# Optimization experiments

Hardware: AMD Instinct MI355X
Metric: run time of the kernel (lower is better)

Reference implementation:

```python
import math
import jax, jax.numpy as jnp
import numpy as np

B, T, C = 4, 2048, 1024
H = 16
D = C // H  # head dim = 64


def setup_inputs() -> dict:
    key = jax.random.key(0)
    ks = jax.random.split(key, 9)
    s = 0.02
    return {
        "x": jax.random.normal(ks[0], (B, T, C), dtype=jnp.float32),
        "Wq": jax.random.normal(ks[1], (C, C), dtype=jnp.float32) * s,
        "bq": jax.random.normal(ks[2], (C,), dtype=jnp.float32) * s,
        "Wk": jax.random.normal(ks[3], (C, C), dtype=jnp.float32) * s,
        "bk": jax.random.normal(ks[4], (C,), dtype=jnp.float32) * s,
        "Wv": jax.random.normal(ks[5], (C, C), dtype=jnp.float32) * s,
        "bv": jax.random.normal(ks[6], (C,), dtype=jnp.float32) * s,
        "Wo": jax.random.normal(ks[7], (C, C), dtype=jnp.float32) * s,
        "bo": jax.random.normal(ks[8], (C,), dtype=jnp.float32) * s,
    }


def reference(x, Wq, bq, Wk, bk, Wv, bv, Wo, bo):
    # Linear projections (torch Linear: x @ W.T + b), split into heads -> [B,H,T,D]
    def heads(y):
        return y.reshape(B, T, H, D).transpose(0, 2, 1, 3)

    q = heads(x @ Wq.T + bq)
    k = heads(x @ Wk.T + bk)
    v = heads(x @ Wv.T + bv)

    # Full [B,H,T,T] score matrix, scaled by 1/sqrt(D) (no mask, dropout=0 / eval)
    scores = jnp.einsum("bhqd,bhkd->bhqk", q, k) / math.sqrt(D)
    attn = jax.nn.softmax(scores, axis=-1)
    out = jnp.einsum("bhqk,bhkd->bhqd", attn, v)
    out = out.transpose(0, 2, 1, 3).reshape(B, T, C)
    return out @ Wo.T + bo
```

## Files before the change

kernel.cpp:

```cpp
#include <hip/hip_runtime.h>
#include <hip/hip_bf16.h>
#include <stdint.h>

#define Bb 4
#define Tt 2048
#define Cc 1024
#define Hh 16
#define Dd 64

using bf16x8 = __bf16 __attribute__((ext_vector_type(8)));
using f32x4  = float  __attribute__((ext_vector_type(4)));
using f32x2  = float  __attribute__((ext_vector_type(2)));
typedef short s16x4 __attribute__((ext_vector_type(4)));
typedef unsigned short u16;
typedef unsigned int   u32;

#if defined(__has_builtin) && __has_builtin(__builtin_amdgcn_mfma_f32_16x16x16bf16_1k)
#define MFMA_16x16x16_BF16(a, b, c) __builtin_amdgcn_mfma_f32_16x16x16bf16_1k(a, b, c, 0, 0, 0)
#else
static __device__ __forceinline__ f32x4 mfma16x16x16bf16_asm(s16x4 a, s16x4 b, f32x4 c) {
  f32x4 d;
  asm volatile("v_mfma_f32_16x16x16_bf16 %0, %1, %2, %3" : "=v"(d) : "v"(a), "v"(b), "v"(c));
  return d;
}
#define MFMA_16x16x16_BF16(a, b, c) mfma16x16x16bf16_asm(a, b, c)
#endif

#if defined(__has_builtin) && __has_builtin(__builtin_amdgcn_exp2f)
#define EXP2F(x) __builtin_amdgcn_exp2f(x)
#else
#define EXP2F(x) exp2f(x)
#endif

__device__ __forceinline__ u16 f32_to_bf16(float f) {
  union { float f; unsigned u; } v; v.f = f;
  unsigned r = v.u + 0x7fffu + ((v.u >> 16) & 1u);
  return (u16)(r >> 16);
}

__device__ __forceinline__ void gl2lds16(const u16* g, u16* l) {
  __builtin_amdgcn_global_load_lds(
      (const __attribute__((address_space(1))) u32*)g,
      (__attribute__((address_space(3))) u32*)l, 16, 0, 0);
}

__global__ void cast_f32_to_bf16(const float* __restrict__ in, u16* __restrict__ out, int n) {
  int i = (blockIdx.x * blockDim.x + threadIdx.x) * 4;
  if (i >= n) return;
  float4 v = *reinterpret_cast<const float4*>(in + i);
  ushort4 o;
  o.x = f32_to_bf16(v.x); o.y = f32_to_bf16(v.y);
  o.z = f32_to_bf16(v.z); o.w = f32_to_bf16(v.w);
  *reinterpret_cast<ushort4*>(out + i) = o;
}

__global__ void cast4_f32_to_bf16(const float* __restrict__ w0, const float* __restrict__ w1,
                                  const float* __restrict__ w2, const float* __restrict__ w3,
                                  u16* __restrict__ o0, u16* __restrict__ o1,
                                  u16* __restrict__ o2, u16* __restrict__ o3, int n) {
  const float* in; u16* out;
  switch (blockIdx.y) {
    case 0: in = w0; out = o0; break;
    case 1: in = w1; out = o1; break;
    case 2: in = w2; out = o2; break;
    default: in = w3; out = o3; break;
  }
  int i = (blockIdx.x * blockDim.x + threadIdx.x) * 4;
  if (i >= n) return;
  float4 v = *reinterpret_cast<const float4*>(in + i);
  ushort4 o;
  o.x = f32_to_bf16(v.x); o.y = f32_to_bf16(v.y);
  o.z = f32_to_bf16(v.z); o.w = f32_to_bf16(v.w);
  *reinterpret_cast<ushort4*>(out + i) = o;
}

__global__ __launch_bounds__(256, 2)
void gemm_qkv(const u16* __restrict__ A, const u16* __restrict__ Bqkv,
              const float* __restrict__ bq, const float* __restrict__ bk,
              const float* __restrict__ bv,
              u16* __restrict__ qout, u16* __restrict__ kout, u16* __restrict__ vtout,
              float qscl)
{
  constexpr int K = Cc, BK = 32, LDT = 136;
  __shared__ alignas(16) u16 smem[128 * LDT];
  u16* As = smem;
  u16* Bs = smem + 128 * BK;
  const int tid  = threadIdx.x;
  const int wave = tid >> 6, lane = tid & 63;
  const int row0 = blockIdx.x * 128, col0 = blockIdx.y * 128;
  const int seg  = col0 >> 10;
  const int wm = (wave & 1) * 64, wn = (wave >> 1) * 64;
  const int fr = lane & 15, fk = (lane >> 4) * 8;
  const int srow = lane >> 2, scol = (lane & 3) * 8;

  f32x4 acc[4][4] = {};

  for (int k0 = 0; k0 < K; k0 += BK) {
#pragma unroll
    for (int c = 0; c < 2; ++c) {
      int rg = (wave * 2 + c) * 16;
      gl2lds16(A    + (size_t)(row0 + rg + srow) * K + k0 + scol, &As[rg * BK]);
      gl2lds16(Bqkv + (size_t)(col0 + rg + srow) * K + k0 + scol, &Bs[rg * BK]);
    }
    __syncthreads();
    bf16x8 af[4], bf[4];
#pragma unroll
    for (int i = 0; i < 4; ++i) {
      af[i] = *reinterpret_cast<const bf16x8*>(&As[(wm + i * 16 + fr) * BK + fk]);
      bf[i] = *reinterpret_cast<const bf16x8*>(&Bs[(wn + i * 16 + fr) * BK + fk]);
    }
#pragma unroll
    for (int i = 0; i < 4; ++i)
#pragma unroll
      for (int j = 0; j < 4; ++j)
        acc[i][j] = __builtin_amdgcn_mfma_f32_16x16x32_bf16(af[i], bf[j], acc[i][j], 0, 0, 0);
    __syncthreads();
  }

  const float* bias = (seg == 0) ? bq : ((seg == 1) ? bk : bv);
  const float scale = (seg == 0) ? qscl : 1.0f;
  const int colL0 = col0 & 1023;

  if (seg < 2) {
    u16* outp = (seg == 0) ? qout : kout;
#pragma unroll
    for (int j = 0; j < 4; ++j) {
      int col = colL0 + wn + j * 16 + fr;
      float bvv = bias[col];
#pragma unroll
      for (int i = 0; i < 4; ++i) {
        int rowb = row0 + wm + i * 16 + (lane >> 4) * 4;
#pragma unroll
        for (int r = 0; r < 4; ++r)
          outp[(size_t)(rowb + r) * Cc + col] = f32_to_bf16((acc[i][j][r] + bvv) * scale);
      }
    }
  } else {
#pragma unroll
    for (int j = 0; j < 4; ++j) {
      int lc = wn + j * 16 + fr;
      float bvv = bias[colL0 + lc];
#pragma unroll
      for (int i = 0; i < 4; ++i) {
        int lr = wm + i * 16 + (lane >> 4) * 4;
#pragma unroll
        for (int r = 0; r < 4; ++r)
          smem[lc * LDT + lr + r] = f32_to_bf16(acc[i][j][r] + bvv);
      }
    }
    __syncthreads();
    int lc = tid >> 1, seg2 = tid & 1;
    int col = colL0 + lc;
    int h = col >> 6, d = col & 63;
    int bb = row0 >> 11, t0 = (row0 & 2047) + seg2 * 64;
    u16* dst = vtout + ((size_t)(bb * Hh + h) * Dd + d) * Tt + t0;
    const u16* src = &smem[lc * LDT + seg2 * 64];
#pragma unroll
    for (int g = 0; g < 8; ++g)
      *reinterpret_cast<uint4*>(dst + g * 8) = *reinterpret_cast<const uint4*>(src + g * 8);
  }
}

__global__ __launch_bounds__(256, 2)
void gemm_out(const u16* __restrict__ A, const u16* __restrict__ Bw,
              const float* __restrict__ bias, float* __restrict__ Cout,
              int M, int N, int K)
{
  constexpr int BK = 32;
  __shared__ alignas(16) u16 As[128 * BK];
  __shared__ alignas(16) u16 Bs[128 * BK];
  const int tid  = threadIdx.x;
  const int wave = tid >> 6, lane = tid & 63;
  const int row0 = blockIdx.x * 128, col0 = blockIdx.y * 128;
  const int wm = (wave & 1) * 64, wn = (wave >> 1) * 64;
  const int fr = lane & 15, fk = (lane >> 4) * 8;
  const int srow = lane >> 2, scol = (lane & 3) * 8;

  f32x4 acc[4][4] = {};

  for (int k0 = 0; k0 < K; k0 += BK) {
#pragma unroll
    for (int c = 0; c < 2; ++c) {
      int rg = (wave * 2 + c) * 16;
      gl2lds16(A  + (size_t)(row0 + rg + srow) * K + k0 + scol, &As[rg * BK]);
      gl2lds16(Bw + (size_t)(col0 + rg + srow) * K + k0 + scol, &Bs[rg * BK]);
    }
    __syncthreads();
    bf16x8 af[4], bf[4];
#pragma unroll
    for (int i = 0; i < 4; ++i) {
      af[i] = *reinterpret_cast<const bf16x8*>(&As[(wm + i * 16 + fr) * BK + fk]);
      bf[i] = *reinterpret_cast<const bf16x8*>(&Bs[(wn + i * 16 + fr) * BK + fk]);
    }
#pragma unroll
    for (int i = 0; i < 4; ++i)
#pragma unroll
      for (int j = 0; j < 4; ++j)
        acc[i][j] = __builtin_amdgcn_mfma_f32_16x16x32_bf16(af[i], bf[j], acc[i][j], 0, 0, 0);
    __syncthreads();
  }

#pragma unroll
  for (int j = 0; j < 4; ++j) {
    int col = col0 + wn + j * 16 + fr;
    float bv = bias[col];
#pragma unroll
    for (int i = 0; i < 4; ++i) {
      int rowb = row0 + wm + i * 16 + (lane >> 4) * 4;
#pragma unroll
      for (int r = 0; r < 4; ++r)
        Cout[(size_t)(rowb + r) * N + col] = acc[i][j][r] + bv;
    }
  }
}

__global__ __launch_bounds__(256, 2)
void attn_kernel(const u16* __restrict__ Q, const u16* __restrict__ Kmat,
                 const u16* __restrict__ VT, u16* __restrict__ O) {
  constexpr int LDK = 72, LDV = 72;
  __shared__ alignas(16) unsigned char smem[18432];
  u16* Ks = (u16*)smem;
  u16* Vs = (u16*)(smem + 9216);
  float* Of = (float*)smem;
  float* Qs = (float*)(smem + 17408);
  const int tid = threadIdx.x, wave = tid >> 6, lane = tid & 63;
  const int bh = blockIdx.x, qt = blockIdx.y;
  const int b = bh >> 4, h = bh & 15;
  const size_t base = (size_t)b * Tt * Cc + (size_t)h * Dd;
  const int fr = lane & 15, qd = lane >> 4;

  bf16x8 bq0[4], bq1[4];
#pragma unroll
  for (int nb = 0; nb < 4; ++nb) {
    const u16* qp = Q + base + (size_t)(qt * 64 + nb * 16 + fr) * Cc + qd * 8;
    bq0[nb] = *reinterpret_cast<const bf16x8*>(qp);
    bq1[nb] = *reinterpret_cast<const bf16x8*>(qp + 32);
  }

  f32x4 Oacc[4][4] = {};
  f32x2 sacc2[4] = {};
  const size_t vtb = (size_t)bh * Dd * Tt;
  const int sr = tid >> 3, sc = (tid & 7) * 8;

  for (int kt = 0; kt < Tt; kt += 64) {
#pragma unroll
    for (int it = 0; it < 2; ++it) {
      int r = it * 32 + sr;
      *reinterpret_cast<uint4*>(&Ks[r * LDK + sc]) =
          *reinterpret_cast<const uint4*>(Kmat + base + (size_t)(kt + r) * Cc + sc);
      *reinterpret_cast<uint4*>(&Vs[r * LDV + sc]) =
          *reinterpret_cast<const uint4*>(VT + vtb + (size_t)r * Tt + kt + sc);
    }
    __syncthreads();

    bf16x8 ka = *reinterpret_cast<const bf16x8*>(&Ks[(wave * 16 + fr) * LDK + qd * 8]);
    bf16x8 kb = *reinterpret_cast<const bf16x8*>(&Ks[(wave * 16 + fr) * LDK + 32 + qd * 8]);
    s16x4 va[4];
#pragma unroll
    for (int n = 0; n < 4; ++n)
      va[n] = *reinterpret_cast<const s16x4*>(&Vs[(n * 16 + fr) * LDV + wave * 16 + qd * 4]);

    s16x4 pf[4];
#pragma unroll
    for (int nb = 0; nb < 4; ++nb) {
      f32x4 z = {};
      z = __builtin_amdgcn_mfma_f32_16x16x32_bf16(ka, bq0[nb], z, 0, 0, 0);
      f32x4 st = __builtin_amdgcn_mfma_f32_16x16x32_bf16(kb, bq1[nb], z, 0, 0, 0);
      float p0 = EXP2F(st[0]), p1 = EXP2F(st[1]);
      float p2 = EXP2F(st[2]), p3 = EXP2F(st[3]);
      sacc2[nb] += (f32x2){p0, p1} + (f32x2){p2, p3};
      union { __hip_bfloat162 h2; short2 s2; } u01, u23;
      u01.h2 = __float22bfloat162_rn(make_float2(p0, p1));
      u23.h2 = __float22bfloat162_rn(make_float2(p2, p3));
      s16x4 pv; pv[0] = u01.s2.x; pv[1] = u01.s2.y;
      pv[2] = u23.s2.x; pv[3] = u23.s2.y;
      pf[nb] = pv;
    }

#pragma unroll
    for (int n = 0; n < 4; ++n)
#pragma unroll
      for (int nb = 0; nb < 4; ++nb)
        Oacc[n][nb] = MFMA_16x16x16_BF16(va[n], pf[nb], Oacc[n][nb]);

    __syncthreads();
  }

#pragma unroll
  for (int nb = 0; nb < 4; ++nb) {
    float s = sacc2[nb][0] + sacc2[nb][1];
    s += __shfl_xor(s, 16, 64);
    s += __shfl_xor(s, 32, 64);
    if (qd == 0) Qs[wave * 64 + nb * 16 + fr] = s;
  }
  for (int w = 0; w < 4; ++w) {
    if (wave == w) {
#pragma unroll
      for (int n = 0; n < 4; ++n)
#pragma unroll
        for (int nb = 0; nb < 4; ++nb) {
          float* dst = &Of[(nb * 16 + fr) * 68 + n * 16 + qd * 4];
          if (w == 0) *reinterpret_cast<f32x4*>(dst) = Oacc[n][nb];
          else {
            f32x4 old = *reinterpret_cast<const f32x4*>(dst);
            *reinterpret_cast<f32x4*>(dst) = old + Oacc[n][nb];
          }
        }
    }
    __syncthreads();
  }

  {
    int q = tid >> 2, dg = tid & 3;
    float qtot = Qs[q] + Qs[64 + q] + Qs[128 + q] + Qs[192 + q];
    float linv = 1.0f / qtot;
    const float* src = &Of[q * 68 + dg * 16];
    alignas(16) u16 tmp[16];
#pragma unroll
    for (int i = 0; i < 16; ++i) tmp[i] = f32_to_bf16(src[i] * linv);
    u16* op = O + base + (size_t)(qt * 64 + q) * Cc + dg * 16;
    *reinterpret_cast<uint4*>(op)     = *reinterpret_cast<const uint4*>(tmp);
    *reinterpret_cast<uint4*>(op + 8) = *reinterpret_cast<const uint4*>(tmp + 8);
  }
}

extern "C" void kernel_launch(void* const* d_in, const int* in_sizes, int n_in,
                              void* d_out, int out_size, void* d_ws, size_t ws_size,
                              hipStream_t stream) {
  const float* x  = (const float*)d_in[0];
  const float* Wq = (const float*)d_in[1];
  const float* bq = (const float*)d_in[2];
  const float* Wk = (const float*)d_in[3];
  const float* bk = (const float*)d_in[4];
  const float* Wv = (const float*)d_in[5];
  const float* bv = (const float*)d_in[6];
  const float* Wo = (const float*)d_in[7];
  const float* bo = (const float*)d_in[8];

  const size_t NX = (size_t)Bb * Tt * Cc;
  const size_t NW = (size_t)Cc * Cc;

  u16* ws  = (u16*)d_ws;
  u16* xb  = ws;
  u16* wqb = ws + NX;
  u16* wkb = wqb + NW;
  u16* wvb = wkb + NW;
  u16* wob = wvb + NW;
  u16* qb  = wob + NW;
  u16* kb  = qb + NX;
  u16* vtb = kb + NX;
  u16* attnb = xb;

  cast_f32_to_bf16<<<(int)(NX / 4 / 256), 256, 0, stream>>>(x, xb, (int)NX);
  cast4_f32_to_bf16<<<dim3((unsigned)(NW / 4 / 256), 4), 256, 0, stream>>>(
      Wq, Wk, Wv, Wo, wqb, wkb, wvb, wob, (int)NW);

  const float QSCL = 0.125f * 1.44269504f;
  gemm_qkv<<<dim3(64, 24), 256, 0, stream>>>(xb, wqb, bq, bk, bv, qb, kb, vtb, QSCL);

  attn_kernel<<<dim3(Bb * Hh, Tt / 64), 256, 0, stream>>>(qb, kb, vtb, attnb);

  gemm_out<<<dim3(64, 8), 256, 0, stream>>>(attnb, wob, bo, (float*)d_out,
                                            Bb * Tt, Cc, Cc);
}
```

Baseline: 303.1 us.

## Switch attention kernel to 32x32x16 MFMA with 128-key tiles and swizzled LDS

Rewrites the attention inner loop around 32x32x16 bf16 MFMA. Each wave now handles 32 keys of a 128-key tile, and the score-to-P layout is fixed up with permlane32_swap instead of using 16x16x16 MFMAs. K and V tiles are stored in XOR-swizzled LDS with no padding, and each barrier now covers a key tile twice as large. The goal is fewer instructions and barriers per key, at the cost of larger LDS use, which may lower occupancy, and a transposed output reduction.

```diff
diff --git a/kernel.cpp b/kernel.cpp
--- a/kernel.cpp
+++ b/kernel.cpp
@@ -10,26 +10,25 @@
 
 using bf16x8 = __bf16 __attribute__((ext_vector_type(8)));
 using f32x4  = float  __attribute__((ext_vector_type(4)));
-using f32x2  = float  __attribute__((ext_vector_type(2)));
-typedef short s16x4 __attribute__((ext_vector_type(4)));
+using f32x16 = float  __attribute__((ext_vector_type(16)));
 typedef unsigned short u16;
 typedef unsigned int   u32;
-
-#if defined(__has_builtin) && __has_builtin(__builtin_amdgcn_mfma_f32_16x16x16bf16_1k)
-#define MFMA_16x16x16_BF16(a, b, c) __builtin_amdgcn_mfma_f32_16x16x16bf16_1k(a, b, c, 0, 0, 0)
-#else
-static __device__ __forceinline__ f32x4 mfma16x16x16bf16_asm(s16x4 a, s16x4 b, f32x4 c) {
-  f32x4 d;
-  asm volatile("v_mfma_f32_16x16x16_bf16 %0, %1, %2, %3" : "=v"(d) : "v"(a), "v"(b), "v"(c));
-  return d;
-}
-#define MFMA_16x16x16_BF16(a, b, c) mfma16x16x16bf16_asm(a, b, c)
-#endif
 
 #if defined(__has_builtin) && __has_builtin(__builtin_amdgcn_exp2f)
 #define EXP2F(x) __builtin_amdgcn_exp2f(x)
 #else
 #define EXP2F(x) exp2f(x)
+#endif
+
+#if defined(__has_builtin) && __has_builtin(__builtin_amdgcn_permlane32_swap)
+#define PERMLANE32_SWAP(a, b)                                          \
+  do {                                                                 \
+    auto _r = __builtin_amdgcn_permlane32_swap((a), (b), false, false);\
+    (a) = _r[0]; (b) = _r[1];                                          \
+  } while (0)
+#else
+#define PERMLANE32_SWAP(a, b) \
+  asm volatile("v_permlane32_swap_b32 %0, %1" : "+v"(a), "+v"(b))
 #endif
 
 __device__ __forceinline__ u16 f32_to_bf16(float f) {
@@ -217,93 +216,122 @@
 __global__ __launch_bounds__(256, 2)
 void attn_kernel(const u16* __restrict__ Q, const u16* __restrict__ Kmat,
                  const u16* __restrict__ VT, u16* __restrict__ O) {
-  constexpr int LDK = 72, LDV = 72;
-  __shared__ alignas(16) unsigned char smem[18432];
+  __shared__ alignas(16) unsigned char smem[32768];
   u16* Ks = (u16*)smem;
-  u16* Vs = (u16*)(smem + 9216);
-  float* Of = (float*)smem;
-  float* Qs = (float*)(smem + 17408);
+  u16* Vs = (u16*)(smem + 16384);
+  float* OfT = (float*)smem;
+  float* Qs  = (float*)(smem + 17408);
+
   const int tid = threadIdx.x, wave = tid >> 6, lane = tid & 63;
-  const int bh = blockIdx.x, qt = blockIdx.y;
+  const int l31 = lane & 31, hi = lane >> 5;
+  const int bh = blockIdx.x, qt0 = blockIdx.y;
   const int b = bh >> 4, h = bh & 15;
   const size_t base = (size_t)b * Tt * Cc + (size_t)h * Dd;
-  const int fr = lane & 15, qd = lane >> 4;
-
-  bf16x8 bq0[4], bq1[4];
-#pragma unroll
-  for (int nb = 0; nb < 4; ++nb) {
-    const u16* qp = Q + base + (size_t)(qt * 64 + nb * 16 + fr) * Cc + qd * 8;
-    bq0[nb] = *reinterpret_cast<const bf16x8*>(qp);
-    bq1[nb] = *reinterpret_cast<const bf16x8*>(qp + 32);
-  }
-
-  f32x4 Oacc[4][4] = {};
-  f32x2 sacc2[4] = {};
   const size_t vtb = (size_t)bh * Dd * Tt;
-  const int sr = tid >> 3, sc = (tid & 7) * 8;
-
-  for (int kt = 0; kt < Tt; kt += 64) {
-#pragma unroll
-    for (int it = 0; it < 2; ++it) {
-      int r = it * 32 + sr;
-      *reinterpret_cast<uint4*>(&Ks[r * LDK + sc]) =
-          *reinterpret_cast<const uint4*>(Kmat + base + (size_t)(kt + r) * Cc + sc);
-      *reinterpret_cast<uint4*>(&Vs[r * LDV + sc]) =
-          *reinterpret_cast<const uint4*>(VT + vtb + (size_t)r * Tt + kt + sc);
-    }
-    __syncthreads();
-
-    bf16x8 ka = *reinterpret_cast<const bf16x8*>(&Ks[(wave * 16 + fr) * LDK + qd * 8]);
-    bf16x8 kb = *reinterpret_cast<const bf16x8*>(&Ks[(wave * 16 + fr) * LDK + 32 + qd * 8]);
-    s16x4 va[4];
-#pragma unroll
-    for (int n = 0; n < 4; ++n)
-      va[n] = *reinterpret_cast<const s16x4*>(&Vs[(n * 16 + fr) * LDV + wave * 16 + qd * 4]);
-
-    s16x4 pf[4];
-#pragma unroll
-    for (int nb = 0; nb < 4; ++nb) {
-      f32x4 z = {};
-      z = __builtin_amdgcn_mfma_f32_16x16x32_bf16(ka, bq0[nb], z, 0, 0, 0);
-      f32x4 st = __builtin_amdgcn_mfma_f32_16x16x32_bf16(kb, bq1[nb], z, 0, 0, 0);
-      float p0 = EXP2F(st[0]), p1 = EXP2F(st[1]);
-      float p2 = EXP2F(st[2]), p3 = EXP2F(st[3]);
-      sacc2[nb] += (f32x2){p0, p1} + (f32x2){p2, p3};
-      union { __hip_bfloat162 h2; short2 s2; } u01, u23;
-      u01.h2 = __float22bfloat162_rn(make_float2(p0, p1));
-      u23.h2 = __float22bfloat162_rn(make_float2(p2, p3));
-      s16x4 pv; pv[0] = u01.s2.x; pv[1] = u01.s2.y;
-      pv[2] = u23.s2.x; pv[3] = u23.s2.y;
-      pf[nb] = pv;
-    }
-
-#pragma unroll
-    for (int n = 0; n < 4; ++n)
-#pragma unroll
-      for (int nb = 0; nb < 4; ++nb)
-        Oacc[n][nb] = MFMA_16x16x16_BF16(va[n], pf[nb], Oacc[n][nb]);
-
-    __syncthreads();
-  }
-
-#pragma unroll
-  for (int nb = 0; nb < 4; ++nb) {
-    float s = sacc2[nb][0] + sacc2[nb][1];
-    s += __shfl_xor(s, 16, 64);
+
+  bf16x8 qb[2][4];
+#pragma unroll
+  for (int qt = 0; qt < 2; ++qt) {
+    const u16* qp = Q + base + (size_t)(qt0 * 64 + qt * 32 + l31) * Cc + hi * 8;
+#pragma unroll
+    for (int c = 0; c < 4; ++c)
+      qb[qt][c] = *reinterpret_cast<const bf16x8*>(qp + c * 16);
+  }
+
+  f32x16 Oacc[2][2] = {};
+  float ssum[2] = {0.f, 0.f};
+
+  const int skey = tid >> 1, sd0 = (tid & 1) * 32;
+  const int svd = tid >> 2, svc = tid & 3;
+
+  for (int kt = 0; kt < Tt; kt += 128) {
+#pragma unroll
+    for (int i = 0; i < 4; ++i) {
+      int d0 = sd0 + i * 8;
+      uint4 kv = *reinterpret_cast<const uint4*>(Kmat + base + (size_t)(kt + skey) * Cc + d0);
+      *reinterpret_cast<uint4*>(&Ks[skey * 64 + (((d0 >> 3) ^ (skey & 7)) << 3)]) = kv;
+      int c = svc + i * 4;
+      uint4 vv = *reinterpret_cast<const uint4*>(VT + vtb + (size_t)svd * Tt + kt + c * 8);
+      *reinterpret_cast<uint4*>(&Vs[svd * 128 + ((c ^ (svd & 15)) << 3)]) = vv;
+    }
+    __syncthreads();
+
+    bf16x8 ka[4], vb[2][2];
+    const int key = wave * 32 + l31;
+#pragma unroll
+    for (int c = 0; c < 4; ++c)
+      ka[c] = *reinterpret_cast<const bf16x8*>(
+          &Ks[key * 64 + ((((c << 1) + hi) ^ (key & 7)) << 3)]);
+#pragma unroll
+    for (int k0i = 0; k0i < 2; ++k0i)
+#pragma unroll
+      for (int dh = 0; dh < 2; ++dh) {
+        int drow = dh * 32 + l31;
+        int ch = wave * 4 + k0i * 2 + hi;
+        vb[k0i][dh] = *reinterpret_cast<const bf16x8*>(
+            &Vs[drow * 128 + ((ch ^ (drow & 15)) << 3)]);
+      }
+
+#pragma unroll
+    for (int qt = 0; qt < 2; ++qt) {
+      f32x16 s = {};
+#pragma unroll
+      for (int c = 0; c < 4; ++c)
+        s = __builtin_amdgcn_mfma_f32_32x32x16_bf16(ka[c], qb[qt][c], s, 0, 0, 0);
+      unsigned pk[8];
+      float sm = 0.f;
+#pragma unroll
+      for (int i = 0; i < 8; ++i) {
+        float p0 = EXP2F(s[2 * i]), p1 = EXP2F(s[2 * i + 1]);
+        sm += p0 + p1;
+        union { __hip_bfloat162 h2; unsigned u; } cv;
+        cv.h2 = __float22bfloat162_rn(make_float2(p0, p1));
+        pk[i] = cv.u;
+      }
+      ssum[qt] += sm;
+      unsigned a0 = pk[0], a1 = pk[1], a2 = pk[2], a3 = pk[3];
+      unsigned b0 = pk[4], b1 = pk[5], b2 = pk[6], b3 = pk[7];
+      PERMLANE32_SWAP(a0, a2);
+      PERMLANE32_SWAP(a1, a3);
+      PERMLANE32_SWAP(b0, b2);
+      PERMLANE32_SWAP(b1, b3);
+      union { unsigned u[4]; bf16x8 v; } plo, phi;
+      plo.u[0] = a0; plo.u[1] = a1; plo.u[2] = a2; plo.u[3] = a3;
+      phi.u[0] = b0; phi.u[1] = b1; phi.u[2] = b2; phi.u[3] = b3;
+      Oacc[qt][0] = __builtin_amdgcn_mfma_f32_32x32x16_bf16(plo.v, vb[0][0], Oacc[qt][0], 0, 0, 0);
+      Oacc[qt][1] = __builtin_amdgcn_mfma_f32_32x32x16_bf16(plo.v, vb[0][1], Oacc[qt][1], 0, 0, 0);
+      Oacc[qt][0] = __builtin_amdgcn_mfma_f32_32x32x16_bf16(phi.v, vb[1][0], Oacc[qt][0], 0, 0, 0);
+      Oacc[qt][1] = __builtin_amdgcn_mfma_f32_32x32x16_bf16(phi.v, vb[1][1], Oacc[qt][1], 0, 0, 0);
+    }
+    __syncthreads();
+  }
+
+#pragma unroll
+  for (int qt = 0; qt < 2; ++qt) {
+    float s = ssum[qt];
     s += __shfl_xor(s, 32, 64);
-    if (qd == 0) Qs[wave * 64 + nb * 16 + fr] = s;
-  }
+    if (hi == 0) Qs[wave * 64 + qt * 32 + l31] = s;
+  }
+
   for (int w = 0; w < 4; ++w) {
     if (wave == w) {
 #pragma unroll
-      for (int n = 0; n < 4; ++n)
-#pragma unroll
-        for (int nb = 0; nb < 4; ++nb) {
-          float* dst = &Of[(nb * 16 + fr) * 68 + n * 16 + qd * 4];
-          if (w == 0) *reinterpret_cast<f32x4*>(dst) = Oacc[n][nb];
-          else {
-            f32x4 old = *reinterpret_cast<const f32x4*>(dst);
-            *reinterpret_cast<f32x4*>(dst) = old + Oacc[n][nb];
+      for (int qt = 0; qt < 2; ++qt)
+#pragma unroll
+        for (int dh = 0; dh < 2; ++dh) {
+          int d = dh * 32 + l31;
+          float* rowp = &OfT[d * 68 + qt * 32 + hi * 4];
+#pragma unroll
+          for (int g = 0; g < 4; ++g) {
+            f32x4 v;
+            v[0] = Oacc[qt][dh][g * 4 + 0]; v[1] = Oacc[qt][dh][g * 4 + 1];
+            v[2] = Oacc[qt][dh][g * 4 + 2]; v[3] = Oacc[qt][dh][g * 4 + 3];
+            float* dst = rowp + g * 8;
+            if (w == 0) *reinterpret_cast<f32x4*>(dst) = v;
+            else {
+              f32x4 old = *reinterpret_cast<const f32x4*>(dst);
+              *reinterpret_cast<f32x4*>(dst) = old + v;
+            }
           }
         }
     }
@@ -314,11 +342,11 @@
     int q = tid >> 2, dg = tid & 3;
     float qtot = Qs[q] + Qs[64 + q] + Qs[128 + q] + Qs[192 + q];
     float linv = 1.0f / qtot;
-    const float* src = &Of[q * 68 + dg * 16];
     alignas(16) u16 tmp[16];
 #pragma unroll
-    for (int i = 0; i < 16; ++i) tmp[i] = f32_to_bf16(src[i] * linv);
-    u16* op = O + base + (size_t)(qt * 64 + q) * Cc + dg * 16;
+    for (int i = 0; i < 16; ++i)
+      tmp[i] = f32_to_bf16(OfT[(dg * 16 + i) * 68 + q] * linv);
+    u16* op = O + base + (size_t)(qt0 * 64 + q) * Cc + dg * 16;
     *reinterpret_cast<uint4*>(op)     = *reinterpret_cast<const uint4*>(tmp);
     *reinterpret_cast<uint4*>(op + 8) = *reinterpret_cast<const uint4*>(tmp + 8);
   }
```

Result: no change. 307.4 us (+1.4%).
